# Kernel optimization log

Measured on AMD Instinct MI355X. Metric: run time of the kernel, lower is better.

Reference implementation:

```python
import jax, jax.numpy as jnp
import numpy as np

T_STEPS = 15          # SpykeTorch time dimension
THR1, THR2 = 15.0, 10.0   # conv1_threshold, conv2_threshold
KWTA2, RADIUS2 = 8, 1     # conv2_kwta, conv2_inhibition_radius


def conv2d(x, w):
    # F.conv2d, no padding, stride 1 (snn.Convolution)
    return jax.lax.conv_general_dilated(
        x, w, window_strides=(1, 1), padding='VALID',
        dimension_numbers=('NCHW', 'OIHW', 'NCHW'))


def maxpool(x, k, s):
    # sf.pooling == F.max_pool2d
    return jax.lax.reduce_window(x, -jnp.inf, jax.lax.max,
                                 (1, 1, k, k), (1, 1, s, s), 'VALID')


def fire(pot, thr):
    # sf.fire with return_thresholded_potentials=True
    pot_t = jnp.where(pot < thr, 0.0, pot)
    return jnp.sign(pot_t), pot_t


def pointwise_inhibition(pot):
    # sf.pointwise_inhibition: at each (h,w) keep only the feature that had the
    # max potential at the time of the earliest spike there.
    T, F, H, W = pot.shape
    max_vals = pot.max(axis=1, keepdims=True)            # (T,1,H,W)
    max_idx = pot.argmax(axis=1)                         # (T,H,W)
    clamp = jnp.sign(max_vals)                           # (T,1,H,W) 0/1 spike flag
    # earliest spike time per position (spikes are cumulative over T)
    earliest = jnp.clip((T - clamp.sum(axis=0)).astype(jnp.int32), 0, T - 1)  # (1,H,W)
    win_ch = jnp.take_along_axis(max_idx, earliest, axis=0)  # (1,H,W)
    # coef: one-hot over feature dim at winner channel, gated by spike at last step
    coef = (jnp.arange(F)[None, :, None, None] == win_ch[:, None, :, :]).astype(pot.dtype)
    coef = coef * clamp[-1:]                              # (1,F,H,W)
    return pot * coef


def get_k_winners(pot, spikes, kwta, radius):
    # sf.get_k_winners: rank by (earliest spike time, potential), then kwta
    # sequential suppression (same feature fully + spatial window, NMS-like).
    T, F, H, W = pot.shape
    first = jnp.clip((T - spikes.sum(axis=0, keepdims=True)).astype(jnp.int32), 0, T - 1)
    values = jnp.take_along_axis(pot, first, axis=0)      # (1,F,H,W)
    trunc = spikes * values
    v = trunc.max() * T                                   # big constant to prioritize early spikes
    total = (trunc + spikes * v).sum(axis=0)              # (F,H,W)
    fr = jnp.arange(F)[:, None, None]
    rr = jnp.arange(H)[None, :, None]
    cc = jnp.arange(W)[None, None, :]
    winners = []
    for _ in range(kwta):  # fixed small loop (kwta=8)
        idx = jnp.argmax(total)
        mx = total.reshape(-1)[idx]
        valid = mx != 0
        f = idx // (H * W)
        rem = idx % (H * W)
        r = rem // W
        c = rem % W
        winners.append(jnp.where(valid, jnp.stack([f, r, c]), -1))
        feat_hit = (fr == f)
        win_hit = (jnp.abs(rr - r) <= radius) & (jnp.abs(cc - c) <= radius)
        total = jnp.where(valid & (feat_hit | win_hit), 0.0, total)
    return jnp.stack(winners).astype(jnp.int32)           # (kwta,3)


def setup_inputs() -> dict:
    key = jax.random.key(0)
    k1, k2, k3 = jax.random.split(key, 3)
    inp = jax.random.randint(k1, (T_STEPS, 6, 160, 160), 0, 2, dtype=jnp.int32)
    # snn.Convolution weights ~ N(mean=0.8, std=0.05)
    w1 = 0.8 + 0.05 * jax.random.normal(k2, (30, 6, 5, 5), dtype=jnp.float32)
    w2 = 0.8 + 0.05 * jax.random.normal(k3, (250, 30, 3, 3), dtype=jnp.float32)
    return {"input": inp, "w1": w1, "w2": w2, "max_layer": 2}


def reference(input, w1, w2, max_layer):
    # Training-mode forward with max_layer == 2 (conv2 training branch).
    x = jnp.pad(input.astype(jnp.float32), ((0, 0), (0, 0), (2, 2), (2, 2)))
    pot = conv2d(x, w1)                                   # (15,30,160,160)
    spk, pot = fire(pot, THR1)
    spk_in = jnp.pad(maxpool(spk, 2, 2), ((0, 0), (0, 0), (1, 1), (1, 1)))
    pot = conv2d(spk_in, w2)                              # (15,250,80,80)
    spk, pot = fire(pot, THR2)
    pot = pointwise_inhibition(pot)
    spk = jnp.sign(pot)
    winners = get_k_winners(pot, spk, KWTA2, RADIUS2)
    return spk, pot, winners
```

## Files before the change

kernel.cpp:

```cpp
#include <hip/hip_runtime.h>


typedef unsigned short u16;
typedef unsigned char u8;
typedef __attribute__((ext_vector_type(8))) short short8;
typedef __attribute__((ext_vector_type(4))) float f32x4;
typedef __attribute__((ext_vector_type(4))) float float4v;

#define T_STEPS 15

#define INPCL_OFF   0u
#define SPKCL_OFF   6612480u
#define SPKROW_OFF  13067520u
#define W1CL_OFF    19119120u
#define WHI_OFF     19139600u
#define WLO_OFF     19287056u
#define MAXV_OFF    19434512u
#define ARGM_OFF    19818512u
#define WINMAP_OFF  20202512u
#define POTWIN_OFF  20228112u
#define CNT_OFF     20612112u
#define RSTHR_OFF   20813840u
#define RSMETA_OFF  20814864u
#define VALG_OFF    20814880u
#define META_OFF    20840480u
#define PMAX_OFF    20866080u

#define NB_REPACK 1615
#define NB_W1     40
#define NB_W2     288
#define NB_BORD   76
#define NB_BROW   18
#define NB_MISC   2
#define PREP_GRID (NB_REPACK + NB_W1 + NB_W2 + NB_BORD + NB_BROW + NB_MISC)

#define NB_CONV1  1500
#define NB_FILL   2048
#define K1B_GRID  (NB_CONV1 + NB_FILL)

#define NB_BMFMA  75
#define WS_GRID   (NB_BMFMA + 375)

static __device__ __forceinline__ u16 f2bf_rne(float f) {
  unsigned u = __float_as_uint(f);
  unsigned r = u + 0x7FFFu + ((u >> 16) & 1u);
  return (u16)(r >> 16);
}
static __device__ __forceinline__ float bf2f(u16 b) {
  return __uint_as_float(((unsigned)b) << 16);
}

static __device__ __forceinline__ void ring_decode(int r, int& h, int& w) {
  if (r < 80) { h = 0; w = r; }
  else if (r < 160) { h = 79; w = r - 80; }
  else if (r < 238) { h = 1 + (r - 160); w = 0; }
  else { h = 1 + (r - 238); w = 79; }
}

__global__ __launch_bounds__(256) void prep_kernel(
    const int* __restrict__ xin, const float* __restrict__ w1,
    const float* __restrict__ w2, u16* __restrict__ inp_cl,
    u16* __restrict__ w1cl, u16* __restrict__ Whi, u16* __restrict__ Wlo,
    u16* __restrict__ spk_cl, u16* __restrict__ spk_row,
    u16* __restrict__ cnt, float* __restrict__ rs_thr,
    float* __restrict__ rsmeta) {
  int tid = threadIdx.x, b = blockIdx.x;

  if (b < NB_REPACK) {
    int g = b * 256 + tid;
    if (g < 413280) {
      int t = g / 27552, rem = g % 27552;
      int yy = rem / 168, xx = rem % 168;
      int y = yy - 2, x = xx - 2;
      short8 sv = {0, 0, 0, 0, 0, 0, 0, 0};
      if ((unsigned)y < 160u && (unsigned)x < 160u) {
        const int* xb = xin + ((size_t)t * 6 * 160 + y) * 160 + x;
#pragma unroll
        for (int c = 0; c < 6; ++c)
          sv[c] = xb[c * 25600] ? (short)0x3F80 : (short)0;
      }
      *(short8*)(inp_cl + (size_t)g * 8) = sv;
    }
  } else if (b < NB_REPACK + NB_W1) {
    int idx = (b - NB_REPACK) * 256 + tid;
    int f = idx / 320, r = idx % 320;
    int ky = r / 64, r2 = r % 64;
    int kxb = r2 >> 5, k = r2 & 31;
    int dx = k >> 3, c = k & 7;
    int kx = kxb * 4 + dx;
    u16 v = 0;
    if (f < 30 && c < 6 && kx < 5)
      v = f2bf_rne(w1[(f * 6 + c) * 25 + ky * 5 + kx]);
    w1cl[idx] = v;
  } else if (b < NB_REPACK + NB_W1 + NB_W2) {
    int g2 = (b - NB_REPACK - NB_W1) * 256 + tid;
    int f = g2 / 288, r = g2 % 288;
    int kk = r >> 5, c = r & 31;
    u16 h = 0, l = 0;
    if (f < 250 && c < 30) {
      float w = w2[f * 270 + c * 9 + kk];
      h = f2bf_rne(w);
      l = f2bf_rne(w - bf2f(h));
    }
    Whi[g2] = h;
    Wlo[g2] = l;
  } else if (b < NB_REPACK + NB_W1 + NB_W2 + NB_BORD) {
    int u = (b - NB_REPACK - NB_W1 - NB_W2) * 256 + tid;
    if (u < 19440) {
      int pid = u >> 2, part = u & 3;
      int t = pid / 324, i = pid % 324;
      int row, col;
      if (i < 82) { row = 0; col = i; }
      else if (i < 164) { row = 81; col = i - 82; }
      else if (i < 244) { row = 1 + (i - 164); col = 0; }
      else { row = 1 + (i - 244); col = 81; }
      short8 z = {0, 0, 0, 0, 0, 0, 0, 0};
      *(short8*)(spk_cl + (((size_t)t * 82 + row) * 82 + col) * 32 +
                 part * 8) = z;
    }
  } else if (b < NB_REPACK + NB_W1 + NB_W2 + NB_BORD + NB_BROW) {
    int u0 = (b - NB_REPACK - NB_W1 - NB_W2 - NB_BORD) * 256 + tid;
    for (int v = u0; v < 145800; v += NB_BROW * 256) {
      int tc = v / 324, i = v % 324;
      int row, col;
      if (i < 82) { row = 0; col = i; }
      else if (i < 164) { row = 81; col = i - 82; }
      else if (i < 244) { row = 1 + (i - 164); col = 0; }
      else { row = 1 + (i - 244); col = 81; }
      spk_row[(size_t)tc * 6724 + row * 82 + col] = 0;
    }
  } else if (b == NB_REPACK + NB_W1 + NB_W2 + NB_BORD + NB_BROW) {
    __shared__ float sv[256];
    __shared__ int si[256];
    float a = 0.f;
    if (tid < 250) {
      const float* wt = w2 + tid * 270;
      for (int c = 0; c < 30; ++c)
#pragma unroll
        for (int kk = 0; kk < 9; ++kk)
          a = fmaf(wt[c * 9 + kk], 1.0f, a);
    }
    float thr = (a >= 10.f) ? a : 0.f;
    if (tid < 250) rs_thr[tid] = thr;
    sv[tid] = (tid < 250) ? thr : -1.f;
    si[tid] = tid;
    __syncthreads();
    for (int s = 128; s > 0; s >>= 1) {
      if (tid < s) {
        if (sv[tid + s] > sv[tid] ||
            (sv[tid + s] == sv[tid] && si[tid + s] < si[tid])) {
          sv[tid] = sv[tid + s];
          si[tid] = si[tid + s];
        }
      }
      __syncthreads();
    }
    if (tid == 0) {
      rsmeta[0] = sv[0];
      ((int*)rsmeta)[1] = si[0];
    }
  } else {
    for (int i = tid; i < 4860; i += 256) {
      int t = i / 324, r = i % 324;
      int row, col;
      if (r < 82) { row = 0; col = r; }
      else if (r < 164) { row = 81; col = r - 82; }
      else if (r < 244) { row = 1 + (r - 164); col = 0; }
      else { row = 1 + (r - 244); col = 81; }
      cnt[t * 6724 + row * 82 + col] = 0;
    }
  }
}

__global__ __launch_bounds__(256) void conv1_fill_kernel(
    const u16* __restrict__ inp_cl, const u16* __restrict__ w1cl,
    u16* __restrict__ spk_cl, u16* __restrict__ spk_row,
    u16* __restrict__ cnt, float4v* __restrict__ out4, int out_n4) {
  __shared__ __align__(16) u16 tile[20 * 24 * 8];
  __shared__ u8 fires[30 * 256];
  __shared__ u16 pooled[64 * 32];

  int tid = threadIdx.x, b = blockIdx.x;

  if (b >= NB_CONV1) {
    int i = (b - NB_CONV1) * 256 + tid;
    float4v z = {0.f, 0.f, 0.f, 0.f};
    for (; i < out_n4; i += NB_FILL * 256) out4[i] = z;
    return;
  }

  int t = b / 100, tile_id = b % 100;
  int ty0 = (tile_id / 10) * 16, tx0 = (tile_id % 10) * 16;
  int lane = tid & 63, wave = tid >> 6, lrow = lane & 15, lgrp = lane >> 4;

  const u16* ib = inp_cl + (size_t)t * 164 * 168 * 8;
  for (int i = tid; i < 480; i += 256) {
    int row = i / 24, col = i % 24;
    *(short8*)&tile[i * 8] =
        *(const short8*)(ib + (((ty0 + row) * 168) + tx0 + col) * 8);
  }

  short8 afr[2][10];
#pragma unroll
  for (int mt = 0; mt < 2; ++mt)
#pragma unroll
    for (int s = 0; s < 10; ++s)
      afr[mt][s] =
          *(const short8*)(w1cl + ((mt * 16 + lrow) * 10 + s) * 32 + lgrp * 8);

  __syncthreads();

  for (int ph = 0; ph < 4; ++ph) {
    int rrow = ph * 4 + wave;
    f32x4 acc0 = {0.f, 0.f, 0.f, 0.f}, acc1 = {0.f, 0.f, 0.f, 0.f};
#pragma unroll
    for (int s = 0; s < 10; ++s) {
      int ky = s >> 1, kxb = s & 1;
      short8 bfr = *(const short8*)&tile[
          ((rrow + ky) * 24 + lrow + kxb * 4 + lgrp) * 8];
      acc0 = __builtin_amdgcn_mfma_f32_16x16x32_bf16(afr[0][s], bfr, acc0,
                                                     0, 0, 0);
      acc1 = __builtin_amdgcn_mfma_f32_16x16x32_bf16(afr[1][s], bfr, acc1,
                                                     0, 0, 0);
    }
#pragma unroll
    for (int r = 0; r < 4; ++r) {
      int f0 = lgrp * 4 + r;
      fires[f0 * 256 + rrow * 16 + lrow] = (acc0[r] >= 15.f);
      int f1 = 16 + lgrp * 4 + r;
      if (f1 < 30) fires[f1 * 256 + rrow * 16 + lrow] = (acc1[r] >= 15.f);
    }
  }
  __syncthreads();

  int pby0 = (ty0 >> 1) + 1, pbx0 = (tx0 >> 1) + 1;

  for (int idx = tid; idx < 2048; idx += 256) {
    int f = idx >> 6, pp = idx & 63;
    int py = pp >> 3, px = pp & 7;
    u16 v = 0;
    if (f < 30) {
      const u8* fb = &fires[f * 256 + py * 32 + px * 2];
      v = (fb[0] | fb[1] | fb[16] | fb[17]) ? (u16)0x3F80 : (u16)0;
    }
    pooled[pp * 32 + f] = v;
  }
  for (int idx = tid; idx < 1920; idx += 256) {
    int f = idx >> 6, pp = idx & 63;
    int py = pp >> 3, px = pp & 7;
    const u8* fb = &fires[f * 256 + py * 32 + px * 2];
    u16 v = (fb[0] | fb[1] | fb[16] | fb[17]) ? (u16)0x3F80 : (u16)0;
    spk_row[((t * 30 + f) * 82 + pby0 + py) * 82 + pbx0 + px] = v;
  }
  __syncthreads();

  int pos = tid >> 2, part = tid & 3;
  int yy = pby0 + (pos >> 3), xx = pbx0 + (pos & 7);
  *(short8*)(spk_cl + (((size_t)t * 82 + yy) * 82 + xx) * 32 + part * 8) =
      *(short8*)&pooled[pos * 32 + part * 8];

  if (tid < 64) {
    int c = 0;
#pragma unroll
    for (int f = 0; f < 30; ++f) c += (pooled[tid * 32 + f] != 0) ? 1 : 0;
    cnt[t * 6724 + (pby0 + (tid >> 3)) * 82 + (pbx0 + (tid & 7))] = (u16)c;
  }
}

__global__ __launch_bounds__(256) void winsparse_kernel(
    const u16* __restrict__ spk_cl, const u16* __restrict__ spk_row,
    const u16* __restrict__ cnt, const u16* __restrict__ Whi,
    const u16* __restrict__ Wlo, const float* __restrict__ w2,
    const float* __restrict__ rsmeta, float* __restrict__ maxv_ws,
    int* __restrict__ argm_ws) {
  int tid = threadIdx.x, b = blockIdx.x;

  if (b >= NB_BMFMA) {
    int g = (b - NB_BMFMA) * 256 + tid;
    int t = g / 6400, pos = g % 6400;
    int h = pos / 80, w = pos % 80;
    if (h == 0 || h == 79 || w == 0 || w == 79) return;
    const u16* cb = cnt + t * 6724;
    int W = 0;
#pragma unroll
    for (int ky = 0; ky < 3; ++ky) {
      const u16* r = cb + (h + ky) * 82 + w;
      W += r[0] + r[1] + r[2];
    }
    if (W == 270) {
      maxv_ws[g] = rsmeta[0];
      argm_ws[g] = ((const int*)rsmeta)[1];
    } else {
      const u16* srb = spk_row + (size_t)t * 30 * 6724;
      float bv = -1.f; int bf = 0;
      for (int f = 0; f < 250; ++f) {
        const float* wt = w2 + f * 270;
        float a = 0.f;
        for (int c = 0; c < 30; ++c)
#pragma unroll
          for (int ky = 0; ky < 3; ++ky)
#pragma unroll
            for (int kx = 0; kx < 3; ++kx)
              a = fmaf(wt[c * 9 + ky * 3 + kx],
                       bf2f(srb[c * 6724 + (h + ky) * 82 + (w + kx)]), a);
        float v = (a >= 10.f) ? a : 0.f;
        if (v > bv) { bv = v; bf = f; }
      }
      maxv_ws[g] = bv;
      argm_ws[g] = bf;
    }
    return;
  }

  __shared__ __align__(16) u16 Xt[64 * 320];
  __shared__ int eid[64];

  if (tid < 64) {
    int e = b * 64 + tid;
    if (e >= 4740) e = 4739;
    int t = e / 316, r = e % 316;
    int h, w;
    ring_decode(r, h, w);
    eid[tid] = t * 6400 + h * 80 + w;
  }
  __syncthreads();

  for (int task = tid; task < 2304; task += 256) {
    int e = task / 36, r = task % 36;
    int kk = r >> 2, part = r & 3;
    int g = eid[e];
    int t = g / 6400, pos = g % 6400;
    int h = pos / 80, w = pos % 80;
    int ky = kk / 3, kx = kk % 3;
    short8 v = *(const short8*)(
        spk_cl + (((size_t)t * 82 + h + ky) * 82 + (w + kx)) * 32 + part * 8);
    int off = (e * 320 + kk * 32 + part * 8) ^ ((e & 7) << 3);
    *(short8*)(Xt + off) = v;
  }
  __syncthreads();

  int lane = tid & 63, wave = tid >> 6, lrow = lane & 15, lgrp = lane >> 4;
  int fbase = wave * 64;

  f32x4 acc[4][4];
#pragma unroll
  for (int i = 0; i < 4; ++i)
#pragma unroll
    for (int j = 0; j < 4; ++j) acc[i][j] = (f32x4){0.f, 0.f, 0.f, 0.f};

  const u16* whib = Whi + (fbase + lrow) * 288 + lgrp * 8;
  const u16* wlob = Wlo + (fbase + lrow) * 288 + lgrp * 8;
  int xorr = (lrow & 7) << 3;

#pragma unroll
  for (int ks = 0; ks < 9; ++ks) {
    short8 ahi[4], alo[4], bfr[4];
#pragma unroll
    for (int ft = 0; ft < 4; ++ft) {
      ahi[ft] = *(const short8*)(whib + ft * 16 * 288 + ks * 32);
      alo[ft] = *(const short8*)(wlob + ft * 16 * 288 + ks * 32);
    }
#pragma unroll
    for (int pt = 0; pt < 4; ++pt) {
      int s = ((pt * 16 + lrow) * 320 + ks * 32 + lgrp * 8) ^ xorr;
      bfr[pt] = *(const short8*)(Xt + s);
    }
#pragma unroll
    for (int ft = 0; ft < 4; ++ft)
#pragma unroll
      for (int pt = 0; pt < 4; ++pt) {
        acc[ft][pt] = __builtin_amdgcn_mfma_f32_16x16x32_bf16(
            ahi[ft], bfr[pt], acc[ft][pt], 0, 0, 0);
        acc[ft][pt] = __builtin_amdgcn_mfma_f32_16x16x32_bf16(
            alo[ft], bfr[pt], acc[ft][pt], 0, 0, 0);
      }
  }

  __syncthreads();
  float* redv = (float*)Xt;
  int* redi = (int*)(Xt + 512);

#pragma unroll
  for (int pt = 0; pt < 4; ++pt) {
    float bv = -1.f; int bf = 0;
#pragma unroll
    for (int ft = 0; ft < 4; ++ft)
#pragma unroll
      for (int r = 0; r < 4; ++r) {
        float v = acc[ft][pt][r];
        v = (v >= 10.f) ? v : 0.f;
        int f = fbase + ft * 16 + lgrp * 4 + r;
        if (v > bv) { bv = v; bf = f; }
      }
    {
      float ov = __shfl_xor(bv, 16); int of = __shfl_xor(bf, 16);
      if (ov > bv || (ov == bv && of < bf)) { bv = ov; bf = of; }
      ov = __shfl_xor(bv, 32); of = __shfl_xor(bf, 32);
      if (ov > bv || (ov == bv && of < bf)) { bv = ov; bf = of; }
    }
    if (lgrp == 0) {
      redv[wave * 64 + pt * 16 + lrow] = bv;
      redi[wave * 64 + pt * 16 + lrow] = bf;
    }
  }
  __syncthreads();
  if (tid < 64) {
    float bv = -1.f; int bf = 0x7fffffff;
#pragma unroll
    for (int w = 0; w < 4; ++w) {
      float v = redv[w * 64 + tid]; int f = redi[w * 64 + tid];
      if (v > bv || (v == bv && f < bf)) { bv = v; bf = f; }
    }
    int g = eid[tid];
    maxv_ws[g] = bv;
    argm_ws[g] = bf;
  }
}

__global__ __launch_bounds__(256) void recompute_kernel(
    const u16* __restrict__ spk_row, const float* __restrict__ w2,
    const u16* __restrict__ cnt, const float* __restrict__ rs_thr,
    const float* __restrict__ maxv, const int* __restrict__ argm,
    int* __restrict__ winmap, float* __restrict__ potwin,
    float* __restrict__ out) {
  __shared__ u16 patch[30 * 18 * 18];
  __shared__ int anyp;

  int tid = threadIdx.x, b = blockIdx.x;
  int t = b / 25, tile = b % 25;
  int ty0 = (tile / 5) * 16, tx0 = (tile % 5) * 16;
  int py = tid >> 4, px = tid & 15;
  int h = ty0 + py, w = tx0 + px;
  int pos = h * 80 + w;

  const u16* cb = cnt + t * 6724;
  int W = 0;
#pragma unroll
  for (int ky = 0; ky < 3; ++ky) {
    const u16* r = cb + (h + ky) * 82 + w;
    W += r[0] + r[1] + r[2];
  }
  int partial = (W != 270);
  if (tid == 0) anyp = 0;
  __syncthreads();
  if (partial) anyp = 1;
  __syncthreads();
  int do_stage = anyp;

  if (do_stage) {
    const u16* base = spk_row + (size_t)t * 30 * 6724;
    unsigned* p32 = (unsigned*)patch;
    for (int idx = tid; idx < 4860; idx += 256) {
      int c = idx / 162, rem = idx % 162;
      int dy = rem / 9, dxp = rem % 9;
      p32[idx] = *(const unsigned*)(base + c * 6724 + (ty0 + dy) * 82 + tx0 +
                                    dxp * 2);
    }
  }

  int nc = 0;
#pragma unroll
  for (int tt = 0; tt < T_STEPS; ++tt)
    nc += (maxv[tt * 6400 + pos] > 0.f) ? 1 : 0;
  int e = T_STEPS - nc; if (e > 14) e = 14;
  int win = argm[e * 6400 + pos];
  if (!(maxv[14 * 6400 + pos] > 0.f)) win = -1;
  if (t == 0) winmap[pos] = win;

  if (do_stage) __syncthreads();

  float p = 0.f;
  if (win >= 0) {
    if (!partial) {
      p = rs_thr[win];
    } else {
      const float* wt = w2 + win * 270;
      float a = 0.f;
      for (int c = 0; c < 30; ++c) {
#pragma unroll
        for (int ky = 0; ky < 3; ++ky)
#pragma unroll
          for (int kx = 0; kx < 3; ++kx)
            a = fmaf(wt[c * 9 + ky * 3 + kx],
                     bf2f(patch[c * 324 + (py + ky) * 18 + (px + kx)]), a);
      }
      p = (a >= 10.f) ? a : 0.f;
    }
  }
  potwin[t * 6400 + pos] = p;

  if (win >= 0) {
    int o = (t * 250 + win) * 6400 + pos;
    out[o] = (p > 0.f) ? 1.f : 0.f;
    out[24000000 + o] = p;
  }
}

__global__ __launch_bounds__(256) void prefin_kernel(
    const int* __restrict__ winmap, const float* __restrict__ potwin,
    float* __restrict__ valg, int* __restrict__ meta,
    float* __restrict__ pmax) {
  __shared__ float red[256];

  int tid = threadIdx.x, b = blockIdx.x;
  int pos = b * 256 + tid;

  int win = winmap[pos];
  float val = 0.f; int nspk = 0;
  if (win >= 0) {
#pragma unroll
    for (int t = 0; t < T_STEPS; ++t)
      nspk += (potwin[t * 6400 + pos] > 0.f) ? 1 : 0;
    int first = T_STEPS - nspk; if (first > 14) first = 14;
    val = potwin[first * 6400 + pos];
  }
  valg[pos] = val;
  meta[pos] = ((win + 1) << 4) | nspk;

  red[tid] = (win >= 0 && nspk > 0) ? val : 0.f;
  __syncthreads();
  for (int s = 128; s > 0; s >>= 1) {
    if (tid < s) red[tid] = fmaxf(red[tid], red[tid + s]);
    __syncthreads();
  }
  if (tid == 0) pmax[b] = red[0];
}

__global__ __launch_bounds__(1024) void finalize_kernel(
    const float* __restrict__ valg, const int* __restrict__ meta,
    const float* __restrict__ pmax, float* __restrict__ out_win) {
  __shared__ float tv[6400];
  __shared__ int   tf[6400];
  __shared__ float wv_s[16];
  __shared__ int   wk_s[16];
  __shared__ int   sh_w[4];
  __shared__ float vmax_s;

  int tid = threadIdx.x;
  int lane = tid & 63, wid = tid >> 6;

  if (tid == 0) {
    float m = 0.f;
#pragma unroll
    for (int i = 0; i < 25; ++i) m = fmaxf(m, pmax[i]);
    vmax_s = m * (float)T_STEPS;
  }
  __syncthreads();
  float v = vmax_s;

  for (int pos = tid; pos < 6400; pos += 1024) {
    int me = meta[pos];
    int win = (me >> 4) - 1, nspk = me & 15;
    tf[pos] = win;
    tv[pos] = (win >= 0) ? (float)nspk * (valg[pos] + v) : 0.f;
  }
  __syncthreads();

  for (int it = 0; it < 8; ++it) {
    float bv = -1.f; int bk = 0x7fffffff;
    for (int pos = tid; pos < 6400; pos += 1024) {
      float tvv = tv[pos];
      int key = tf[pos] * 6400 + pos;
      if (tvv > bv || (tvv == bv && key < bk)) { bv = tvv; bk = key; }
    }
#pragma unroll
    for (int m = 1; m < 64; m <<= 1) {
      float ov = __shfl_xor(bv, m); int ok = __shfl_xor(bk, m);
      if (ov > bv || (ov == bv && ok < bk)) { bv = ov; bk = ok; }
    }
    if (lane == 0) { wv_s[wid] = bv; wk_s[wid] = bk; }
    __syncthreads();
    if (tid == 0) {
      float mbv = -1.f; int mbk = 0x7fffffff;
#pragma unroll
      for (int w = 0; w < 16; ++w) {
        float ov = wv_s[w]; int ok = wk_s[w];
        if (ov > mbv || (ov == mbv && ok < mbk)) { mbv = ov; mbk = ok; }
      }
      int f = -1, r = -1, c = -1, valid = 0;
      if (mbv != 0.f) {
        f = mbk / 6400; int pos = mbk % 6400;
        r = pos / 80; c = pos % 80;
        valid = 1;
      }
      out_win[it * 3 + 0] = (float)f;
      out_win[it * 3 + 1] = (float)r;
      out_win[it * 3 + 2] = (float)c;
      sh_w[0] = f; sh_w[1] = r; sh_w[2] = c; sh_w[3] = valid;
    }
    __syncthreads();
    if (sh_w[3]) {
      int wf = sh_w[0], wr = sh_w[1], wc = sh_w[2];
      for (int pos = tid; pos < 6400; pos += 1024) {
        int r = pos / 80, c = pos % 80;
        int dr = r - wr; if (dr < 0) dr = -dr;
        int dc = c - wc; if (dc < 0) dc = -dc;
        if (tf[pos] == wf || (dr <= 1 && dc <= 1)) tv[pos] = 0.f;
      }
    }
    __syncthreads();
  }
}

extern "C" void kernel_launch(void* const* d_in, const int* in_sizes, int n_in,
                              void* d_out, int out_size, void* d_ws,
                              size_t ws_size, hipStream_t stream) {
  const int*   xin = (const int*)d_in[0];
  const float* w1  = (const float*)d_in[1];
  const float* w2  = (const float*)d_in[2];
  float* out = (float*)d_out;
  char*  ws  = (char*)d_ws;

  u16*   inp_cl  = (u16*)(ws + INPCL_OFF);
  u16*   spk_cl  = (u16*)(ws + SPKCL_OFF);
  u16*   spk_row = (u16*)(ws + SPKROW_OFF);
  u16*   w1cl    = (u16*)(ws + W1CL_OFF);
  u16*   Whi     = (u16*)(ws + WHI_OFF);
  u16*   Wlo     = (u16*)(ws + WLO_OFF);
  float* maxv    = (float*)(ws + MAXV_OFF);
  int*   argm    = (int*)(ws + ARGM_OFF);
  int*   winmap  = (int*)(ws + WINMAP_OFF);
  float* potwin  = (float*)(ws + POTWIN_OFF);
  u16*   cnt     = (u16*)(ws + CNT_OFF);
  float* rs_thr  = (float*)(ws + RSTHR_OFF);
  float* rsmeta  = (float*)(ws + RSMETA_OFF);
  float* valg    = (float*)(ws + VALG_OFF);
  int*   meta    = (int*)(ws + META_OFF);
  float* pmax    = (float*)(ws + PMAX_OFF);

  prep_kernel<<<PREP_GRID, 256, 0, stream>>>(xin, w1, w2, inp_cl, w1cl, Whi,
                                             Wlo, spk_cl, spk_row, cnt,
                                             rs_thr, rsmeta);
  conv1_fill_kernel<<<K1B_GRID, 256, 0, stream>>>(inp_cl, w1cl, spk_cl,
                                                  spk_row, cnt,
                                                  (float4v*)d_out,
                                                  out_size / 4);
  winsparse_kernel<<<WS_GRID, 256, 0, stream>>>(spk_cl, spk_row, cnt, Whi,
                                                Wlo, w2, rsmeta, maxv, argm);
  recompute_kernel<<<375, 256, 0, stream>>>(spk_row, w2, cnt, rs_thr, maxv,
                                            argm, winmap, potwin, out);
  prefin_kernel<<<25, 256, 0, stream>>>(winmap, potwin, valg, meta, pmax);
  finalize_kernel<<<1, 1024, 0, stream>>>(valg, meta, pmax, out + 48000000);
}
```

Before: 127.2 us.

## Fuse prep repacking into conv1 kernel, read input and weights directly

Removes the separate prep kernel. The conv1 blocks now build their input tile directly from the int input and repack the conv1 weights into shared memory themselves. The remaining prep duties (w2 split, border zeroing, row-sum threshold) run as extra blocks of the same launch. This drops one kernel launch and the global round trip through the intermediate padded input buffer. In exchange, every conv1 block redundantly converts the weights, and shared memory use per block grows, which may lower occupancy.

```diff
diff --git a/kernel.cpp b/kernel.cpp
--- a/kernel.cpp
+++ b/kernel.cpp
@@ -9,10 +9,8 @@
 
 #define T_STEPS 15
 
-#define INPCL_OFF   0u
 #define SPKCL_OFF   6612480u
 #define SPKROW_OFF  13067520u
-#define W1CL_OFF    19119120u
 #define WHI_OFF     19139600u
 #define WLO_OFF     19287056u
 #define MAXV_OFF    19434512u
@@ -26,17 +24,12 @@
 #define META_OFF    20840480u
 #define PMAX_OFF    20866080u
 
-#define NB_REPACK 1615
-#define NB_W1     40
+#define NB_CONV1  1500
+#define NB_FILL   2048
 #define NB_W2     288
 #define NB_BORD   76
 #define NB_BROW   18
-#define NB_MISC   2
-#define PREP_GRID (NB_REPACK + NB_W1 + NB_W2 + NB_BORD + NB_BROW + NB_MISC)
-
-#define NB_CONV1  1500
-#define NB_FILL   2048
-#define K1B_GRID  (NB_CONV1 + NB_FILL)
+#define K1_GRID   (NB_CONV1 + NB_FILL + NB_W2 + NB_BORD + NB_BROW + 2)
 
 #define NB_BMFMA  75
 #define WS_GRID   (NB_BMFMA + 375)
@@ -49,7 +42,6 @@
 static __device__ __forceinline__ float bf2f(u16 b) {
   return __uint_as_float(((unsigned)b) << 16);
 }
-
 static __device__ __forceinline__ void ring_decode(int r, int& h, int& w) {
   if (r < 80) { h = 0; w = r; }
   else if (r < 160) { h = 79; w = r - 80; }
@@ -57,32 +49,125 @@
   else { h = 1 + (r - 238); w = 79; }
 }
 
-__global__ __launch_bounds__(256) void prep_kernel(
+__global__ __launch_bounds__(256) void conv1_aux_kernel(
     const int* __restrict__ xin, const float* __restrict__ w1,
-    const float* __restrict__ w2, u16* __restrict__ inp_cl,
-    u16* __restrict__ w1cl, u16* __restrict__ Whi, u16* __restrict__ Wlo,
-    u16* __restrict__ spk_cl, u16* __restrict__ spk_row,
-    u16* __restrict__ cnt, float* __restrict__ rs_thr,
-    float* __restrict__ rsmeta) {
+    const float* __restrict__ w2, u16* __restrict__ spk_cl,
+    u16* __restrict__ spk_row, u16* __restrict__ cnt,
+    u16* __restrict__ Whi, u16* __restrict__ Wlo,
+    float* __restrict__ rs_thr, float* __restrict__ rsmeta,
+    float4v* __restrict__ out4, int out_n4) {
+  __shared__ __align__(16) u16 tile[20 * 24 * 8];
+  __shared__ __align__(16) u16 w1s[10240];
+  __shared__ u8 fires[30 * 256];
+  __shared__ u16 pooled[64 * 32];
+  __shared__ float sv[256];
+  __shared__ int si[256];
+
   int tid = threadIdx.x, b = blockIdx.x;
 
-  if (b < NB_REPACK) {
-    int g = b * 256 + tid;
-    if (g < 413280) {
-      int t = g / 27552, rem = g % 27552;
-      int yy = rem / 168, xx = rem % 168;
-      int y = yy - 2, x = xx - 2;
-      short8 sv = {0, 0, 0, 0, 0, 0, 0, 0};
-      if ((unsigned)y < 160u && (unsigned)x < 160u) {
-        const int* xb = xin + ((size_t)t * 6 * 160 + y) * 160 + x;
-#pragma unroll
-        for (int c = 0; c < 6; ++c)
-          sv[c] = xb[c * 25600] ? (short)0x3F80 : (short)0;
-      }
-      *(short8*)(inp_cl + (size_t)g * 8) = sv;
-    }
-  } else if (b < NB_REPACK + NB_W1) {
-    int idx = (b - NB_REPACK) * 256 + tid;
+  if (b >= NB_CONV1) {
+    int rb = b - NB_CONV1;
+    if (rb < NB_FILL) {
+      int i = rb * 256 + tid;
+      float4v z = {0.f, 0.f, 0.f, 0.f};
+      for (; i < out_n4; i += NB_FILL * 256) out4[i] = z;
+    } else if (rb < NB_FILL + NB_W2) {
+      int g2 = (rb - NB_FILL) * 256 + tid;
+      int f = g2 / 288, r = g2 % 288;
+      int kk = r >> 5, c = r & 31;
+      u16 h = 0, l = 0;
+      if (f < 250 && c < 30) {
+        float w = w2[f * 270 + c * 9 + kk];
+        h = f2bf_rne(w);
+        l = f2bf_rne(w - bf2f(h));
+      }
+      Whi[g2] = h;
+      Wlo[g2] = l;
+    } else if (rb < NB_FILL + NB_W2 + NB_BORD) {
+      int u = (rb - NB_FILL - NB_W2) * 256 + tid;
+      if (u < 19440) {
+        int pid = u >> 2, part = u & 3;
+        int t = pid / 324, i = pid % 324;
+        int row, col;
+        if (i < 82) { row = 0; col = i; }
+        else if (i < 164) { row = 81; col = i - 82; }
+        else if (i < 244) { row = 1 + (i - 164); col = 0; }
+        else { row = 1 + (i - 244); col = 81; }
+        short8 z = {0, 0, 0, 0, 0, 0, 0, 0};
+        *(short8*)(spk_cl + (((size_t)t * 82 + row) * 82 + col) * 32 +
+                   part * 8) = z;
+      }
+    } else if (rb < NB_FILL + NB_W2 + NB_BORD + NB_BROW) {
+      int u0 = (rb - NB_FILL - NB_W2 - NB_BORD) * 256 + tid;
+      for (int v = u0; v < 145800; v += NB_BROW * 256) {
+        int tc = v / 324, i = v % 324;
+        int row, col;
+        if (i < 82) { row = 0; col = i; }
+        else if (i < 164) { row = 81; col = i - 82; }
+        else if (i < 244) { row = 1 + (i - 164); col = 0; }
+        else { row = 1 + (i - 244); col = 81; }
+        spk_row[(size_t)tc * 6724 + row * 82 + col] = 0;
+      }
+    } else if (rb == NB_FILL + NB_W2 + NB_BORD + NB_BROW) {
+      float a = 0.f;
+      if (tid < 250) {
+        const float* wt = w2 + tid * 270;
+        for (int c = 0; c < 30; ++c)
+#pragma unroll
+          for (int kk = 0; kk < 9; ++kk)
+            a = fmaf(wt[c * 9 + kk], 1.0f, a);
+      }
+      float thr = (a >= 10.f) ? a : 0.f;
+      if (tid < 250) rs_thr[tid] = thr;
+      sv[tid] = (tid < 250) ? thr : -1.f;
+      si[tid] = tid;
+      __syncthreads();
+      for (int s = 128; s > 0; s >>= 1) {
+        if (tid < s) {
+          if (sv[tid + s] > sv[tid] ||
+              (sv[tid + s] == sv[tid] && si[tid + s] < si[tid])) {
+            sv[tid] = sv[tid + s];
+            si[tid] = si[tid + s];
+          }
+        }
+        __syncthreads();
+      }
+      if (tid == 0) {
+        rsmeta[0] = sv[0];
+        ((int*)rsmeta)[1] = si[0];
+      }
+    } else {
+      for (int i = tid; i < 4860; i += 256) {
+        int t = i / 324, r = i % 324;
+        int row, col;
+        if (r < 82) { row = 0; col = r; }
+        else if (r < 164) { row = 81; col = r - 82; }
+        else if (r < 244) { row = 1 + (r - 164); col = 0; }
+        else { row = 1 + (r - 244); col = 81; }
+        cnt[t * 6724 + row * 82 + col] = 0;
+      }
+    }
+    return;
+  }
+
+  int t = b / 100, tile_id = b % 100;
+  int ty0 = (tile_id / 10) * 16, tx0 = (tile_id % 10) * 16;
+  int lane = tid & 63, wave = tid >> 6, lrow = lane & 15, lgrp = lane >> 4;
+
+  for (int i = tid; i < 480; i += 256) {
+    int row = i / 24, col = i % 24;
+    int gy = ty0 + row - 2, gx = tx0 + col - 2;
+    short8 vv = {0, 0, 0, 0, 0, 0, 0, 0};
+    if ((unsigned)gy < 160u && (unsigned)gx < 160u) {
+      const int* xb = xin + ((size_t)t * 6 * 160 + gy) * 160 + gx;
+#pragma unroll
+      for (int c = 0; c < 6; ++c)
+        vv[c] = xb[c * 25600] ? (short)0x3F80 : (short)0;
+    }
+    *(short8*)&tile[i * 8] = vv;
+  }
+
+  for (int idx = tid; idx < 10240; idx += 256) {
     int f = idx / 320, r = idx % 320;
     int ky = r / 64, r2 = r % 64;
     int kxb = r2 >> 5, k = r2 & 31;
@@ -91,114 +176,9 @@
     u16 v = 0;
     if (f < 30 && c < 6 && kx < 5)
       v = f2bf_rne(w1[(f * 6 + c) * 25 + ky * 5 + kx]);
-    w1cl[idx] = v;
-  } else if (b < NB_REPACK + NB_W1 + NB_W2) {
-    int g2 = (b - NB_REPACK - NB_W1) * 256 + tid;
-    int f = g2 / 288, r = g2 % 288;
-    int kk = r >> 5, c = r & 31;
-    u16 h = 0, l = 0;
-    if (f < 250 && c < 30) {
-      float w = w2[f * 270 + c * 9 + kk];
-      h = f2bf_rne(w);
-      l = f2bf_rne(w - bf2f(h));
-    }
-    Whi[g2] = h;
-    Wlo[g2] = l;
-  } else if (b < NB_REPACK + NB_W1 + NB_W2 + NB_BORD) {
-    int u = (b - NB_REPACK - NB_W1 - NB_W2) * 256 + tid;
-    if (u < 19440) {
-      int pid = u >> 2, part = u & 3;
-      int t = pid / 324, i = pid % 324;
-      int row, col;
-      if (i < 82) { row = 0; col = i; }
-      else if (i < 164) { row = 81; col = i - 82; }
-      else if (i < 244) { row = 1 + (i - 164); col = 0; }
-      else { row = 1 + (i - 244); col = 81; }
-      short8 z = {0, 0, 0, 0, 0, 0, 0, 0};
-      *(short8*)(spk_cl + (((size_t)t * 82 + row) * 82 + col) * 32 +
-                 part * 8) = z;
-    }
-  } else if (b < NB_REPACK + NB_W1 + NB_W2 + NB_BORD + NB_BROW) {
-    int u0 = (b - NB_REPACK - NB_W1 - NB_W2 - NB_BORD) * 256 + tid;
-    for (int v = u0; v < 145800; v += NB_BROW * 256) {
-      int tc = v / 324, i = v % 324;
-      int row, col;
-      if (i < 82) { row = 0; col = i; }
-      else if (i < 164) { row = 81; col = i - 82; }
-      else if (i < 244) { row = 1 + (i - 164); col = 0; }
-      else { row = 1 + (i - 244); col = 81; }
-      spk_row[(size_t)tc * 6724 + row * 82 + col] = 0;
-    }
-  } else if (b == NB_REPACK + NB_W1 + NB_W2 + NB_BORD + NB_BROW) {
-    __shared__ float sv[256];
-    __shared__ int si[256];
-    float a = 0.f;
-    if (tid < 250) {
-      const float* wt = w2 + tid * 270;
-      for (int c = 0; c < 30; ++c)
-#pragma unroll
-        for (int kk = 0; kk < 9; ++kk)
-          a = fmaf(wt[c * 9 + kk], 1.0f, a);
-    }
-    float thr = (a >= 10.f) ? a : 0.f;
-    if (tid < 250) rs_thr[tid] = thr;
-    sv[tid] = (tid < 250) ? thr : -1.f;
-    si[tid] = tid;
-    __syncthreads();
-    for (int s = 128; s > 0; s >>= 1) {
-      if (tid < s) {
-        if (sv[tid + s] > sv[tid] ||
-            (sv[tid + s] == sv[tid] && si[tid + s] < si[tid])) {
-          sv[tid] = sv[tid + s];
-          si[tid] = si[tid + s];
-        }
-      }
-      __syncthreads();
-    }
-    if (tid == 0) {
-      rsmeta[0] = sv[0];
-      ((int*)rsmeta)[1] = si[0];
-    }
-  } else {
-    for (int i = tid; i < 4860; i += 256) {
-      int t = i / 324, r = i % 324;
-      int row, col;
-      if (r < 82) { row = 0; col = r; }
-      else if (r < 164) { row = 81; col = r - 82; }
-      else if (r < 244) { row = 1 + (r - 164); col = 0; }
-      else { row = 1 + (r - 244); col = 81; }
-      cnt[t * 6724 + row * 82 + col] = 0;
-    }
-  }
-}
-
-__global__ __launch_bounds__(256) void conv1_fill_kernel(
-    const u16* __restrict__ inp_cl, const u16* __restrict__ w1cl,
-    u16* __restrict__ spk_cl, u16* __restrict__ spk_row,
-    u16* __restrict__ cnt, float4v* __restrict__ out4, int out_n4) {
-  __shared__ __align__(16) u16 tile[20 * 24 * 8];
-  __shared__ u8 fires[30 * 256];
-  __shared__ u16 pooled[64 * 32];
-
-  int tid = threadIdx.x, b = blockIdx.x;
-
-  if (b >= NB_CONV1) {
-    int i = (b - NB_CONV1) * 256 + tid;
-    float4v z = {0.f, 0.f, 0.f, 0.f};
-    for (; i < out_n4; i += NB_FILL * 256) out4[i] = z;
-    return;
-  }
-
-  int t = b / 100, tile_id = b % 100;
-  int ty0 = (tile_id / 10) * 16, tx0 = (tile_id % 10) * 16;
-  int lane = tid & 63, wave = tid >> 6, lrow = lane & 15, lgrp = lane >> 4;
-
-  const u16* ib = inp_cl + (size_t)t * 164 * 168 * 8;
-  for (int i = tid; i < 480; i += 256) {
-    int row = i / 24, col = i % 24;
-    *(short8*)&tile[i * 8] =
-        *(const short8*)(ib + (((ty0 + row) * 168) + tx0 + col) * 8);
-  }
+    w1s[idx] = v;
+  }
+  __syncthreads();
 
   short8 afr[2][10];
 #pragma unroll
@@ -206,9 +186,7 @@
 #pragma unroll
     for (int s = 0; s < 10; ++s)
       afr[mt][s] =
-          *(const short8*)(w1cl + ((mt * 16 + lrow) * 10 + s) * 32 + lgrp * 8);
-
-  __syncthreads();
+          *(const short8*)&w1s[((mt * 16 + lrow) * 10 + s) * 32 + lgrp * 8];
 
   for (int ph = 0; ph < 4; ++ph) {
     int rrow = ph * 4 + wave;
@@ -611,10 +589,8 @@
   float* out = (float*)d_out;
   char*  ws  = (char*)d_ws;
 
-  u16*   inp_cl  = (u16*)(ws + INPCL_OFF);
   u16*   spk_cl  = (u16*)(ws + SPKCL_OFF);
   u16*   spk_row = (u16*)(ws + SPKROW_OFF);
-  u16*   w1cl    = (u16*)(ws + W1CL_OFF);
   u16*   Whi     = (u16*)(ws + WHI_OFF);
   u16*   Wlo     = (u16*)(ws + WLO_OFF);
   float* maxv    = (float*)(ws + MAXV_OFF);
@@ -628,13 +604,9 @@
   int*   meta    = (int*)(ws + META_OFF);
   float* pmax    = (float*)(ws + PMAX_OFF);
 
-  prep_kernel<<<PREP_GRID, 256, 0, stream>>>(xin, w1, w2, inp_cl, w1cl, Whi,
-                                             Wlo, spk_cl, spk_row, cnt,
-                                             rs_thr, rsmeta);
-  conv1_fill_kernel<<<K1B_GRID, 256, 0, stream>>>(inp_cl, w1cl, spk_cl,
-                                                  spk_row, cnt,
-                                                  (float4v*)d_out,
-                                                  out_size / 4);
+  conv1_aux_kernel<<<K1_GRID, 256, 0, stream>>>(
+      xin, w1, w2, spk_cl, spk_row, cnt, Whi, Wlo, rs_thr, rsmeta,
+      (float4v*)d_out, out_size / 4);
   winsparse_kernel<<<WS_GRID, 256, 0, stream>>>(spk_cl, spk_row, cnt, Whi,
                                                 Wlo, w2, rsmeta, maxv, argm);
   recompute_kernel<<<375, 256, 0, stream>>>(spk_row, w2, cnt, rs_thr, maxv,
```

New measurement: 142.3 us. +11.8%, slower.
